# Kernel tuning notes

Hardware: AMD Instinct MI355X
Metric: run time of the kernel (lower is better)

Reference implementation:

```python
import jax, jax.numpy as jnp
import numpy as np

HID = 64      # hidden_dim
HEADS = 4     # attention heads
CH = HID // HEADS  # 16 per-head channels
EDIM = 6      # edge_dim
NEG = 0.2     # leaky_relu negative slope


def _glorot(key, shape):
    fan_in, fan_out = shape[0], shape[-1]
    s = np.sqrt(6.0 / (fan_in + fan_out)).astype(np.float32)
    return jax.random.uniform(key, shape, jnp.float32, -s, s)


def setup_inputs() -> dict:
    key = jax.random.key(0)
    ks = iter(jax.random.split(key, 48))
    N, E, T = 100000, 1200000, 20000
    inp = {
        "x": jax.random.normal(next(ks), (N, 7), jnp.float32),
        "pos": jax.random.normal(next(ks), (N, 3), jnp.float32),
        "node_type": jax.random.randint(next(ks), (N,), 0, 2),
        "edge_index": jax.random.randint(next(ks), (2, E), 0, N),
        "edge_attr": jax.random.normal(next(ks), (E, EDIM), jnp.float32),
        "num_tracks": T,
        "hidden_state": jax.random.normal(next(ks), (T, HID), jnp.float32),
        # params
        "type_emb": jax.random.normal(next(ks), (2, 8), jnp.float32),
        "enc_W1": _glorot(next(ks), (18, HID)), "enc_b1": jnp.zeros((HID,), jnp.float32),
        "enc_W2": _glorot(next(ks), (HID, HID)), "enc_b2": jnp.zeros((HID,), jnp.float32),
        "gru_Wi": _glorot(next(ks), (HID, 3 * HID)), "gru_bi": jnp.zeros((3 * HID,), jnp.float32),
        "gru_Wh": _glorot(next(ks), (HID, 3 * HID)), "gru_bh": jnp.zeros((3 * HID,), jnp.float32),
        "dec_W1": _glorot(next(ks), (HID, HID)), "dec_b1": jnp.zeros((HID,), jnp.float32),
        "dec_W2": _glorot(next(ks), (HID, 7)), "dec_b2": jnp.zeros((7,), jnp.float32),
    }
    for g in ("g1", "g2"):
        inp[g + "_Wl"] = _glorot(next(ks), (HID, HID))
        inp[g + "_bl"] = jnp.zeros((HID,), jnp.float32)
        inp[g + "_Wr"] = _glorot(next(ks), (HID, HID))
        inp[g + "_br"] = jnp.zeros((HID,), jnp.float32)
        inp[g + "_We"] = _glorot(next(ks), (EDIM, HID))
        inp[g + "_att"] = _glorot(next(ks), (HEADS, CH))
        inp[g + "_bias"] = jnp.zeros((HID,), jnp.float32)
    return inp


def _segment_softmax(e, seg, n):
    m = jax.ops.segment_max(e, seg, num_segments=n)
    m = jnp.where(jnp.isfinite(m), m, 0.0)
    ex = jnp.exp(e - m[seg])
    s = jax.ops.segment_sum(ex, seg, num_segments=n)
    return ex / (s[seg] + 1e-16)


def _gatv2(h, src, dst, eattr, Wl, bl, Wr, br, We, att, bias):
    N = h.shape[0]
    xl = (h @ Wl + bl).reshape(N, HEADS, CH)
    xr = (h @ Wr + br).reshape(N, HEADS, CH)
    ea = (eattr @ We).reshape(-1, HEADS, CH)
    g = jax.nn.leaky_relu(xl[src] + xr[dst] + ea, NEG)      # [E, H, C]
    e = jnp.einsum('ehc,hc->eh', g, att)                     # [E, H]
    alpha = _segment_softmax(e, dst, N)                      # [E, H]
    msg = xl[src] * alpha[..., None]                         # [E, H, C]
    out = jax.ops.segment_sum(msg, dst, num_segments=N)
    return out.reshape(N, HID) + bias, alpha


def reference(x, pos, node_type, edge_index, edge_attr, num_tracks, hidden_state,
              type_emb, enc_W1, enc_b1, enc_W2, enc_b2,
              g1_Wl, g1_bl, g1_Wr, g1_br, g1_We, g1_att, g1_bias,
              g2_Wl, g2_bl, g2_Wr, g2_br, g2_We, g2_att, g2_bias,
              gru_Wi, gru_bi, gru_Wh, gru_bh,
              dec_W1, dec_b1, dec_W2, dec_b2):
    N = x.shape[0]
    h = jnp.concatenate([x, pos, type_emb[node_type]], axis=-1)
    h = jax.nn.relu(h @ enc_W1 + enc_b1) @ enc_W2 + enc_b2

    # PyG GATv2Conv: add self loops, edge_attr fill_value='mean' (mean of incoming edges)
    src, dst = edge_index[0], edge_index[1]
    deg = jax.ops.segment_sum(jnp.ones(src.shape[0], jnp.float32), dst, num_segments=N)
    loop_attr = jax.ops.segment_sum(edge_attr, dst, num_segments=N) / jnp.maximum(deg, 1.0)[:, None]
    ar = jnp.arange(N)
    src_a = jnp.concatenate([src, ar])
    dst_a = jnp.concatenate([dst, ar])
    eattr_a = jnp.concatenate([edge_attr, loop_attr], axis=0)

    h1, a1 = _gatv2(h, src_a, dst_a, eattr_a, g1_Wl, g1_bl, g1_Wr, g1_br, g1_We, g1_att, g1_bias)
    h1 = jax.nn.relu(h1)
    h2, a2 = _gatv2(h1, src_a, dst_a, eattr_a, g2_Wl, g2_bl, g2_Wr, g2_br, g2_We, g2_att, g2_bias)

    # GRUCell on the first num_tracks nodes
    ht = h2[:num_tracks]
    gi = ht @ gru_Wi + gru_bi
    gh = hidden_state @ gru_Wh + gru_bh
    r = jax.nn.sigmoid(gi[:, :HID] + gh[:, :HID])
    z = jax.nn.sigmoid(gi[:, HID:2 * HID] + gh[:, HID:2 * HID])
    n = jnp.tanh(gi[:, 2 * HID:] + r * gh[:, 2 * HID:])
    new_tracks = (1.0 - z) * n + z * hidden_state

    new_full = jnp.concatenate([new_tracks, h2[num_tracks:]], axis=0)
    out = jax.nn.relu(new_full @ dec_W1 + dec_b1) @ dec_W2 + dec_b2  # [N, 7]
    final = out.at[:, :3].set(pos + out[:, :3])
    final = final.at[:, 3:6].set(x[:, :3] + out[:, 3:6])
    return final, new_full, a1, a2
```

## Files before the change

kernel.cpp:

```cpp
#include <hip/hip_runtime.h>

#define NEG 0.2f
#define LOG2E 1.44269504088896f
typedef unsigned short u16;

__device__ __forceinline__ float sigmoidf_(float v){ return 1.f/(1.f+__expf(-v)); }
__device__ __forceinline__ int rfl_(int v){ return __builtin_amdgcn_readfirstlane(v); }
__device__ __forceinline__ float bf2f_(unsigned u){ return __uint_as_float(u<<16); }
__device__ __forceinline__ u16 f2bf_(float f){
  unsigned u = __float_as_uint(f);
  u += 0x7FFFu + ((u>>16)&1u);
  return (u16)(u>>16);
}
template<int C>
__device__ __forceinline__ float dppadd_(float p){
  int r = __builtin_amdgcn_update_dpp(0, __float_as_int(p), C, 0xF, 0xF, true);
  return p + __int_as_float(r);
}
__device__ __forceinline__ float dppsum16_(float p){
  p = dppadd_<0x121>(p);
  p = dppadd_<0x122>(p);
  p = dppadd_<0x124>(p);
  p = dppadd_<0x128>(p);
  return p;
}

__global__ __launch_bounds__(256) void encdeg_kernel(
    const float* __restrict__ x, const float* __restrict__ pos,
    const int* __restrict__ ntype, const float* __restrict__ temb,
    const float* __restrict__ W1, const float* __restrict__ b1,
    const float* __restrict__ W2, const float* __restrict__ b2,
    float* __restrict__ hout,
    const int* __restrict__ ei, int* __restrict__ deg,
    int encB, int E, int N)
{
  __shared__ float sW1[18*64];
  __shared__ float sW2[4096];
  __shared__ float fT[4][8*20];
  __shared__ float tT[4][8*64];
  if ((int)blockIdx.x >= encB){
    int e = ((int)blockIdx.x - encB)*256 + threadIdx.x;
    if (e < E) atomicAdd(deg + ei[E+e], 1);
    return;
  }
  for (int i=threadIdx.x; i<18*64; i+=256) sW1[i]=W1[i];
  for (int i=threadIdx.x; i<4096; i+=256)  sW2[i]=W2[i];
  __syncthreads();
  int lane = threadIdx.x & 63;
  int wid  = threadIdx.x >> 6;
  int n0 = (blockIdx.x*4 + wid)*8;
  if (n0 >= N) return;
  float b1v=b1[lane], b2v=b2[lane];
  #pragma unroll
  for (int m=0;m<8;m++){
    int n=n0+m; float fv=0.f;
    if (n<N){
      if (lane<7)       fv=x[(size_t)n*7+lane];
      else if (lane<10) fv=pos[(size_t)n*3+lane-7];
      else if (lane<18) fv=temb[ntype[n]*8+lane-10];
    }
    if (lane<20) fT[wid][m*20+lane]=fv;
  }
  float t[8];
  #pragma unroll
  for (int m=0;m<8;m++) t[m]=b1v;
  #pragma unroll 2
  for (int k=0;k<18;k++){
    float w=sW1[k*64+lane];
    #pragma unroll
    for (int m=0;m<8;m++) t[m] += fT[wid][m*20+k]*w;
  }
  #pragma unroll
  for (int m=0;m<8;m++){ t[m]=fmaxf(t[m],0.f); tT[wid][m*64+lane]=t[m]; }
  float o[8];
  #pragma unroll
  for (int m=0;m<8;m++) o[m]=b2v;
  #pragma unroll 2
  for (int k=0;k<64;k++){
    float w=sW2[k*64+lane];
    #pragma unroll
    for (int m=0;m<8;m++) o[m] += tT[wid][m*64+k]*w;
  }
  #pragma unroll
  for (int m=0;m<8;m++){ int n=n0+m; if (n<N) hout[(size_t)n*64+lane]=o[m]; }
}

__global__ __launch_bounds__(256) void alloc_kernel(
    const int* __restrict__ deg, int* __restrict__ offs, int* __restrict__ counter, int N)
{
  __shared__ int wsum[4], woff[4], sbase;
  int lane = threadIdx.x & 63, w = threadIdx.x >> 6;
  int base = blockIdx.x*1024 + threadIdx.x*4;
  int v[4]; int s=0;
  #pragma unroll
  for (int j=0;j<4;j++){ int i=base+j; v[j]=(i<N)?deg[i]:0; s+=v[j]; }
  int inc=s;
  #pragma unroll
  for (int d=1;d<64;d<<=1){ int t=__shfl_up(inc,d); if (lane>=d) inc+=t; }
  if (lane==63) wsum[w]=inc;
  __syncthreads();
  if (threadIdx.x==0){
    woff[0]=0; woff[1]=wsum[0]; woff[2]=wsum[0]+wsum[1]; woff[3]=wsum[0]+wsum[1]+wsum[2];
    sbase = atomicAdd(counter, woff[3]+wsum[3]);
  }
  __syncthreads();
  int excl = sbase + woff[w] + (inc - s);
  #pragma unroll
  for (int j=0;j<4;j++){ int i=base+j; if (i<N) offs[i]=excl; excl+=v[j]; }
}

__global__ __launch_bounds__(256) void xfrmfill_kernel(
    const float* __restrict__ hin,
    const float* __restrict__ Wl, const float* __restrict__ bl,
    const float* __restrict__ Wr, const float* __restrict__ br,
    u16* __restrict__ xlo, u16* __restrict__ xro,
    const int* __restrict__ ei, const float* __restrict__ eattr,
    const int* __restrict__ offs,
    int* __restrict__ cursor, float4* __restrict__ slots,
    int xfB, int E, int N)
{
  __shared__ float hT[4][16*64];
  if ((int)blockIdx.x >= xfB){
    int e = ((int)blockIdx.x - xfB)*256 + threadIdx.x;
    if (e < E){
      int dst = ei[E + e];
      int p = atomicAdd(cursor + dst, 1);
      const float2* ep = (const float2*)(eattr + (size_t)e*6);
      float2 p0=ep[0], p1=ep[1], p2=ep[2];
      float4 a, b;
      a.x = __int_as_float(e); a.y = __int_as_float(ei[e]);
      a.z = p0.x; a.w = p0.y;
      b.x = p1.x; b.y = p1.y; b.z = p2.x; b.w = p2.y;
      unsigned slot = (unsigned)(offs[dst] + p);
      slots[slot*2u]   = a;
      slots[slot*2u+1] = b;
    }
    return;
  }
  int lane=threadIdx.x&63;
  int wid=threadIdx.x>>6;
  int n0=(blockIdx.x*4+wid)*16;
  if (n0>=N) return;
  #pragma unroll
  for (int m=0;m<16;m++){
    int n=n0+m;
    hT[wid][m*64+lane] = (n<N)? hin[(size_t)n*64+lane] : 0.f;
  }
  float blv=bl[lane], brv=br[lane];
  float al[16], ar[16];
  #pragma unroll
  for (int m=0;m<16;m++){ al[m]=blv; ar[m]=brv; }
  #pragma unroll 2
  for (int k=0;k<64;k++){
    float wl=Wl[k*64+lane], wr=Wr[k*64+lane];
    #pragma unroll
    for (int m=0;m<16;m++){
      float hb = hT[wid][m*64+k];
      al[m]+=hb*wl; ar[m]+=hb*wr;
    }
  }
  #pragma unroll
  for (int m=0;m<16;m++){
    int n=n0+m;
    if (n<N){ xlo[(((unsigned)n)<<6)+lane]=f2bf_(al[m]); xro[(((unsigned)n)<<6)+lane]=f2bf_(ar[m]); }
  }
}

__global__ __launch_bounds__(256) void xfrm_kernel(
    const float* __restrict__ hin,
    const float* __restrict__ Wl, const float* __restrict__ bl,
    const float* __restrict__ Wr, const float* __restrict__ br,
    u16* __restrict__ xlo, u16* __restrict__ xro, int N)
{
  __shared__ float sWl[4096], sWr[4096];
  __shared__ float hT[4][16*64];
  for (int i=threadIdx.x;i<4096;i+=256){ sWl[i]=Wl[i]; sWr[i]=Wr[i]; }
  __syncthreads();
  int lane=threadIdx.x&63;
  int wid=threadIdx.x>>6;
  int n0=(blockIdx.x*4+wid)*16;
  if (n0>=N) return;
  #pragma unroll
  for (int m=0;m<16;m++){
    int n=n0+m;
    hT[wid][m*64+lane] = (n<N)? hin[(size_t)n*64+lane] : 0.f;
  }
  float blv=bl[lane], brv=br[lane];
  float al[16], ar[16];
  #pragma unroll
  for (int m=0;m<16;m++){ al[m]=blv; ar[m]=brv; }
  #pragma unroll 2
  for (int k=0;k<64;k++){
    float wl=sWl[k*64+lane], wr=sWr[k*64+lane];
    #pragma unroll
    for (int m=0;m<16;m++){
      float hb = hT[wid][m*64+k];
      al[m]+=hb*wl; ar[m]+=hb*wr;
    }
  }
  #pragma unroll
  for (int m=0;m<16;m++){
    int n=n0+m;
    if (n<N){ xlo[(((unsigned)n)<<6)+lane]=f2bf_(al[m]); xro[(((unsigned)n)<<6)+lane]=f2bf_(ar[m]); }
  }
}

#define EDGE_STEP(EIDX, EADD, XV) do {                                       \
    float s_ = (XV) + xrv + (EADD);                                          \
    s_ = fmaxf(s_, NEG*s_);                                                  \
    float p_ = dppsum16_(s_*attv);                                           \
    if (isbase) aout[(((unsigned)(EIDX))<<2)+h] = p_;                        \
    if (__all(p_ <= mmax)) {                                                 \
      float w_ = exp2f(p_ - mmax);                                           \
      ssum += w_; acc += w_*(XV);                                            \
    } else {                                                                 \
      float mn_ = fmaxf(mmax, p_);                                           \
      float sc_ = exp2f(mmax - mn_);                                         \
      float w_  = exp2f(p_ - mn_);                                           \
      ssum = ssum*sc_ + w_;                                                  \
      acc  = acc*sc_ + w_*(XV);                                              \
      mmax = mn_;                                                            \
    }                                                                        \
  } while(0)

#define EDGE_PRE(J, OO) \
    float4 u##J = slots[(unsigned)(OO)*2u], v##J = slots[(unsigned)(OO)*2u+1u]; \
    int e##J = rfl_(__float_as_int(u##J.x)); \
    int s##J = rfl_(__float_as_int(u##J.y)); \
    unsigned xv##J = xlb[(((unsigned)s##J)<<6)+lane];

#define EDGE_BODY(J) \
    float d##J = u##J.z*we0 + u##J.w*we1 + v##J.x*we2 + v##J.y*we3 + v##J.z*we4 + v##J.w*we5; \
    dsum += d##J; \
    EDGE_STEP(e##J, d##J, bf2f_(xv##J));

__global__ __launch_bounds__(256) void gat_kernel(
    const float4* __restrict__ slots, const int* __restrict__ offs, const int* __restrict__ deg,
    const u16* __restrict__ xlb, const u16* __restrict__ xrb,
    const float* __restrict__ We, const float* __restrict__ att,
    const float* __restrict__ bias,
    float* __restrict__ aout, float2* __restrict__ msbuf,
    float* __restrict__ hout,
    int E, int N, int do_relu)
{
  int lane = threadIdx.x & 63;
  int n = blockIdx.x*4 + (threadIdx.x>>6);
  if (n >= N) return;
  float we0=We[lane], we1=We[64+lane], we2=We[128+lane],
        we3=We[192+lane], we4=We[256+lane], we5=We[320+lane];
  float attv = att[lane] * LOG2E;
  float bv = bias[lane];
  float xrv = bf2f_(xrb[(((unsigned)n)<<6)+lane]);
  int h = lane >> 4;
  bool isbase = (lane & 15) == 0;
  int o0 = rfl_(offs[n]);
  int dg = rfl_(deg[n]);
  int oend = o0 + dg;
  float mmax = -3.402823e38f, ssum=0.f, acc=0.f, dsum=0.f;
  int o = o0;
  for (; o+4 <= oend; o += 4){
    EDGE_PRE(0,o); EDGE_PRE(1,o+1); EDGE_PRE(2,o+2); EDGE_PRE(3,o+3);
    EDGE_BODY(0); EDGE_BODY(1); EDGE_BODY(2); EDGE_BODY(3);
  }
  for (; o < oend; ++o){
    EDGE_PRE(0,o);
    EDGE_BODY(0);
  }
  {
    float dS = dsum * (1.f/fmaxf((float)dg,1.f));
    float xvS = bf2f_((unsigned)xlb[(((unsigned)n)<<6)+lane]);
    EDGE_STEP(E+n, dS, xvS);
  }
  float sinv = 1.f/(ssum + 1e-16f);
  if (isbase) msbuf[(((unsigned)n)<<2)+h] = make_float2(mmax, sinv);
  float outv = acc*sinv + bv;
  if (do_relu) outv = fmaxf(outv, 0.f);
  hout[(((unsigned)n)<<6)+lane] = outv;
}

__global__ __launch_bounds__(256) void grudecalpha_kernel(
    const float* __restrict__ h2, const float* __restrict__ hid,
    const float* __restrict__ Wi, const float* __restrict__ bi,
    const float* __restrict__ Wh, const float* __restrict__ bh,
    const int* __restrict__ Tptr,
    const float* __restrict__ W1, const float* __restrict__ b1,
    const float* __restrict__ W2, const float* __restrict__ b2,
    const float* __restrict__ x, const float* __restrict__ pos,
    float* __restrict__ nf, float* __restrict__ fout,
    const int* __restrict__ ei,
    const float2* __restrict__ ms1, const float2* __restrict__ ms2,
    float4* __restrict__ a1, float4* __restrict__ a2,
    int gdB, int E, int N)
{
  __shared__ float sW1[4096];
  __shared__ float sW2[448];
  __shared__ float sb2[8];
  __shared__ float tT[4][8*68];
  __shared__ float pT[4][8*68];
  if ((int)blockIdx.x >= gdB){
    int e = ((int)blockIdx.x - gdB)*256 + threadIdx.x;
    if (e < E+N){
      int dst = (e<E)? ei[E+e] : (e-E);
      {
        float4 r = a1[e];
        const float2* mp = ms1 + (((unsigned)dst)<<2);
        float2 m0=mp[0], m1=mp[1], m2=mp[2], m3=mp[3];
        float4 o;
        o.x = exp2f(r.x - m0.x)*m0.y;
        o.y = exp2f(r.y - m1.x)*m1.y;
        o.z = exp2f(r.z - m2.x)*m2.y;
        o.w = exp2f(r.w - m3.x)*m3.y;
        a1[e] = o;
      }
      {
        float4 r = a2[e];
        const float2* mp = ms2 + (((unsigned)dst)<<2);
        float2 m0=mp[0], m1=mp[1], m2=mp[2], m3=mp[3];
        float4 o;
        o.x = exp2f(r.x - m0.x)*m0.y;
        o.y = exp2f(r.y - m1.x)*m1.y;
        o.z = exp2f(r.z - m2.x)*m2.y;
        o.w = exp2f(r.w - m3.x)*m3.y;
        a2[e] = o;
      }
    }
    return;
  }
  for (int i=threadIdx.x;i<4096;i+=256) sW1[i]=W1[i];
  for (int i=threadIdx.x;i<448;i+=256) sW2[i]=W2[i];
  if (threadIdx.x<7)  sb2[threadIdx.x]=b2[threadIdx.x];
  __syncthreads();
  int lane = threadIdx.x & 63;
  int wid  = threadIdx.x >> 6;
  int n0 = (blockIdx.x*4 + wid)*8;
  if (n0 >= N) return;
  int T = *Tptr;
  float hv[8], nfv[8];
  #pragma unroll
  for (int m=0;m<8;m++){ int n=n0+m; hv[m] = (n<N)? h2[(size_t)n*64+lane] : 0.f; }
  if (n0 < T){
    float pv[8];
    #pragma unroll
    for (int m=0;m<8;m++){ int n=n0+m; pv[m] = (n<T)? hid[(size_t)n*64+lane] : 0.f; }
    #pragma unroll
    for (int m=0;m<8;m++){ tT[wid][m*68+lane]=hv[m]; pT[wid][m*68+lane]=pv[m]; }
    float gr[8],gz[8],gn[8],hr[8],hz[8],hn[8];
    #pragma unroll
    for (int m=0;m<8;m++){ gr[m]=0.f;gz[m]=0.f;gn[m]=0.f;hr[m]=0.f;hz[m]=0.f;hn[m]=0.f; }
    for (int k=0;k<64;k++){
      float wir=Wi[k*192+lane], wiz=Wi[k*192+64+lane], win=Wi[k*192+128+lane];
      float whr=Wh[k*192+lane], whz=Wh[k*192+64+lane], whn=Wh[k*192+128+lane];
      #pragma unroll
      for (int m=0;m<8;m++){
        float a=tT[wid][m*68+k], b=pT[wid][m*68+k];
        gr[m]+=a*wir; gz[m]+=a*wiz; gn[m]+=a*win;
        hr[m]+=b*whr; hz[m]+=b*whz; hn[m]+=b*whn;
      }
    }
    float bir=bi[lane], biz=bi[64+lane], bin=bi[128+lane];
    float bhr=bh[lane], bhz=bh[64+lane], bhn=bh[128+lane];
    #pragma unroll
    for (int m=0;m<8;m++){
      int n=n0+m;
      if (n<T){
        float r  = sigmoidf_(gr[m]+bir + hr[m]+bhr);
        float z  = sigmoidf_(gz[m]+biz + hz[m]+bhz);
        float nn = tanhf(gn[m]+bin + r*(hn[m]+bhn));
        nfv[m] = (1.f-z)*nn + z*pv[m];
      } else {
        nfv[m] = hv[m];
      }
    }
  } else {
    #pragma unroll
    for (int m=0;m<8;m++) nfv[m] = hv[m];
  }
  #pragma unroll
  for (int m=0;m<8;m++){ int n=n0+m; if (n<N) nf[(size_t)n*64+lane]=nfv[m]; }
  #pragma unroll
  for (int m=0;m<8;m++) tT[wid][m*68+lane]=nfv[m];
  float t[8];
  float b1v=b1[lane];
  #pragma unroll
  for (int m=0;m<8;m++) t[m]=b1v;
  #pragma unroll 2
  for (int k=0;k<64;k++){
    float w=sW1[k*64+lane];
    #pragma unroll
    for (int m=0;m<8;m++) t[m] += tT[wid][m*68+k]*w;
  }
  #pragma unroll
  for (int m=0;m<8;m++) t[m]=fmaxf(t[m],0.f);
  #pragma unroll
  for (int m=0;m<8;m++) tT[wid][m*68+lane]=t[m];
  int mm = lane >> 3, cc = lane & 7;
  if (cc < 7){
    float a2v = sb2[cc];
    #pragma unroll 4
    for (int k=0;k<64;k++) a2v += tT[wid][mm*68+k]*sW2[k*7+cc];
    int n = n0+mm;
    if (n < N){
      if (cc<3)      a2v += pos[(size_t)n*3+cc];
      else if (cc<6) a2v += x[(size_t)n*7+(cc-3)];
      fout[(size_t)n*7+cc] = a2v;
    }
  }
}

extern "C" void kernel_launch(void* const* d_in, const int* in_sizes, int n_in,
                              void* d_out, int out_size, void* d_ws, size_t ws_size,
                              hipStream_t stream)
{
  const float* x     = (const float*)d_in[0];
  const float* pos   = (const float*)d_in[1];
  const int*   ntype = (const int*)d_in[2];
  const int*   eidx  = (const int*)d_in[3];
  const float* eattr = (const float*)d_in[4];
  const int*   Tptr  = (const int*)d_in[5];
  const float* hid   = (const float*)d_in[6];
  const float* temb  = (const float*)d_in[7];
  const float* encW1 = (const float*)d_in[8];
  const float* encb1 = (const float*)d_in[9];
  const float* encW2 = (const float*)d_in[10];
  const float* encb2 = (const float*)d_in[11];
  const float* gruWi = (const float*)d_in[12];
  const float* grubi = (const float*)d_in[13];
  const float* gruWh = (const float*)d_in[14];
  const float* grubh = (const float*)d_in[15];
  const float* decW1 = (const float*)d_in[16];
  const float* decb1 = (const float*)d_in[17];
  const float* decW2 = (const float*)d_in[18];
  const float* decb2 = (const float*)d_in[19];
  const float* gWl[2]  = {(const float*)d_in[20], (const float*)d_in[27]};
  const float* gbl[2]  = {(const float*)d_in[21], (const float*)d_in[28]};
  const float* gWr[2]  = {(const float*)d_in[22], (const float*)d_in[29]};
  const float* gbr[2]  = {(const float*)d_in[23], (const float*)d_in[30]};
  const float* gWe[2]  = {(const float*)d_in[24], (const float*)d_in[31]};
  const float* gatt[2] = {(const float*)d_in[25], (const float*)d_in[32]};
  const float* gbias[2]= {(const float*)d_in[26], (const float*)d_in[33]};

  int N  = in_sizes[0] / 7;
  int E  = in_sizes[3] / 2;
  int Ea = E + N;

  char* w = (char*)d_ws;
  float* A      = (float*)w; w += (size_t)N*64*sizeof(float);
  u16*   XL     = (u16*)w;  w += (size_t)N*64*sizeof(u16);
  u16*   XR     = (u16*)w;  w += (size_t)N*64*sizeof(u16);
  float2* msbuf1= (float2*)w; w += (size_t)N*4*sizeof(float2);
  float2* msbuf2= (float2*)w; w += (size_t)N*4*sizeof(float2);
  float4* slots = (float4*)w; w += (size_t)E*32;
  int*   deg    = (int*)w;   w += (size_t)N*sizeof(int);
  int*   cursor = (int*)w;   w += (size_t)N*sizeof(int);
  int*   counter= (int*)w;   w += 4*sizeof(int);
  int*   offs   = (int*)w;   w += (size_t)N*sizeof(int);

  float* out_final = (float*)d_out;
  float* out_nf    = out_final + (size_t)N*7;
  float* out_a1    = out_nf + (size_t)N*64;
  float* out_a2    = out_a1 + (size_t)Ea*4;

  hipMemsetAsync(deg, 0, ((size_t)2*N + 4)*sizeof(int), stream);

  int encB = (N+31)/32;
  int degB = (E+255)/256;
  encdeg_kernel<<<encB+degB, 256, 0, stream>>>(x,pos,ntype,temb,encW1,encb1,encW2,encb2,A,
      eidx, deg, encB, E, N);

  alloc_kernel<<<(N+1023)/1024, 256, 0, stream>>>(deg, offs, counter, N);

  int xfB = (N+63)/64;
  int flB = (E+255)/256;
  xfrmfill_kernel<<<xfB+flB, 256, 0, stream>>>(A, gWl[0], gbl[0], gWr[0], gbr[0], XL, XR,
      eidx, eattr, offs, cursor, slots, xfB, E, N);

  gat_kernel<<<(N+3)/4, 256, 0, stream>>>(slots, offs, deg, XL, XR,
      gWe[0], gatt[0], gbias[0], out_a1, msbuf1, A, E, N, 1);

  xfrm_kernel<<<xfB, 256, 0, stream>>>(A, gWl[1], gbl[1], gWr[1], gbr[1], XL, XR, N);
  gat_kernel<<<(N+3)/4, 256, 0, stream>>>(slots, offs, deg, XL, XR,
      gWe[1], gatt[1], gbias[1], out_a2, msbuf2, A, E, N, 0);

  int gdB = (N+31)/32;
  int alB = (Ea+255)/256;
  grudecalpha_kernel<<<gdB+alB, 256, 0, stream>>>(A, hid, gruWi, grubi, gruWh, grubh, Tptr,
      decW1, decb1, decW2, decb2, x, pos, out_nf, out_final,
      eidx, msbuf1, msbuf2, (float4*)out_a1, (float4*)out_a2, gdB, E, N);
}
```

Measured before the change: 509.1 us.

## Move layer-1 alpha normalization into xfrm kernel and seed cursor with offsets

The layer-1 attention normalization pass now runs as extra blocks inside the second transform kernel, so the final GRU/decoder kernel only normalizes layer-2 alphas and the two passes spread across two launches. The alloc kernel writes the prefix offsets straight into the cursor array, which lets the fill step take the slot index from the atomic and skip the offs[dst] lookup, and the memset shrinks. The xfrm and decoder kernels also stop staging weights in shared memory and read them from global/cache instead. This is meant to shorten the tail kernel and trim memory traffic, at the risk of slower uncached weight reads in the inner loops.

After: 499.1 us. -2.0%, faster.

```diff
diff --git a/kernel.cpp b/kernel.cpp
--- a/kernel.cpp
+++ b/kernel.cpp
@@ -23,6 +23,22 @@
   p = dppadd_<0x124>(p);
   p = dppadd_<0x128>(p);
   return p;
+}
+
+__device__ __forceinline__ void alpha_body_(int e, const int* __restrict__ ei,
+    const float2* __restrict__ ms, float4* __restrict__ a, int E, int N)
+{
+  if (e >= E+N) return;
+  int dst = (e<E)? ei[E+e] : (e-E);
+  float4 r = a[e];
+  const float2* mp = ms + (((unsigned)dst)<<2);
+  float2 m0=mp[0], m1=mp[1], m2=mp[2], m3=mp[3];
+  float4 o;
+  o.x = exp2f(r.x - m0.x)*m0.y;
+  o.y = exp2f(r.y - m1.x)*m1.y;
+  o.z = exp2f(r.z - m2.x)*m2.y;
+  o.w = exp2f(r.w - m3.x)*m3.y;
+  a[e] = o;
 }
 
 __global__ __launch_bounds__(256) void encdeg_kernel(
@@ -86,7 +102,8 @@
 }
 
 __global__ __launch_bounds__(256) void alloc_kernel(
-    const int* __restrict__ deg, int* __restrict__ offs, int* __restrict__ counter, int N)
+    const int* __restrict__ deg, int* __restrict__ offs, int* __restrict__ cursor,
+    int* __restrict__ counter, int N)
 {
   __shared__ int wsum[4], woff[4], sbase;
   int lane = threadIdx.x & 63, w = threadIdx.x >> 6;
@@ -106,7 +123,11 @@
   __syncthreads();
   int excl = sbase + woff[w] + (inc - s);
   #pragma unroll
-  for (int j=0;j<4;j++){ int i=base+j; if (i<N) offs[i]=excl; excl+=v[j]; }
+  for (int j=0;j<4;j++){
+    int i=base+j;
+    if (i<N){ offs[i]=excl; cursor[i]=excl; }
+    excl+=v[j];
+  }
 }
 
 __global__ __launch_bounds__(256) void xfrmfill_kernel(
@@ -115,7 +136,6 @@
     const float* __restrict__ Wr, const float* __restrict__ br,
     u16* __restrict__ xlo, u16* __restrict__ xro,
     const int* __restrict__ ei, const float* __restrict__ eattr,
-    const int* __restrict__ offs,
     int* __restrict__ cursor, float4* __restrict__ slots,
     int xfB, int E, int N)
 {
@@ -124,14 +144,13 @@
     int e = ((int)blockIdx.x - xfB)*256 + threadIdx.x;
     if (e < E){
       int dst = ei[E + e];
-      int p = atomicAdd(cursor + dst, 1);
+      unsigned slot = (unsigned)atomicAdd(cursor + dst, 1);
       const float2* ep = (const float2*)(eattr + (size_t)e*6);
       float2 p0=ep[0], p1=ep[1], p2=ep[2];
       float4 a, b;
       a.x = __int_as_float(e); a.y = __int_as_float(ei[e]);
       a.z = p0.x; a.w = p0.y;
       b.x = p1.x; b.y = p1.y; b.z = p2.x; b.w = p2.y;
-      unsigned slot = (unsigned)(offs[dst] + p);
       slots[slot*2u]   = a;
       slots[slot*2u+1] = b;
     }
@@ -166,16 +185,20 @@
   }
 }
 
-__global__ __launch_bounds__(256) void xfrm_kernel(
+__global__ __launch_bounds__(256) void xfrmalpha_kernel(
     const float* __restrict__ hin,
     const float* __restrict__ Wl, const float* __restrict__ bl,
     const float* __restrict__ Wr, const float* __restrict__ br,
-    u16* __restrict__ xlo, u16* __restrict__ xro, int N)
-{
-  __shared__ float sWl[4096], sWr[4096];
+    u16* __restrict__ xlo, u16* __restrict__ xro,
+    const int* __restrict__ ei, const float2* __restrict__ ms1, float4* __restrict__ a1,
+    int xfB, int E, int N)
+{
   __shared__ float hT[4][16*64];
-  for (int i=threadIdx.x;i<4096;i+=256){ sWl[i]=Wl[i]; sWr[i]=Wr[i]; }
-  __syncthreads();
+  if ((int)blockIdx.x >= xfB){
+    int e = ((int)blockIdx.x - xfB)*256 + threadIdx.x;
+    alpha_body_(e, ei, ms1, a1, E, N);
+    return;
+  }
   int lane=threadIdx.x&63;
   int wid=threadIdx.x>>6;
   int n0=(blockIdx.x*4+wid)*16;
@@ -191,7 +214,7 @@
   for (int m=0;m<16;m++){ al[m]=blv; ar[m]=brv; }
   #pragma unroll 2
   for (int k=0;k<64;k++){
-    float wl=sWl[k*64+lane], wr=sWr[k*64+lane];
+    float wl=Wl[k*64+lane], wr=Wr[k*64+lane];
     #pragma unroll
     for (int m=0;m<16;m++){
       float hb = hT[wid][m*64+k];
@@ -288,45 +311,18 @@
     const float* __restrict__ x, const float* __restrict__ pos,
     float* __restrict__ nf, float* __restrict__ fout,
     const int* __restrict__ ei,
-    const float2* __restrict__ ms1, const float2* __restrict__ ms2,
-    float4* __restrict__ a1, float4* __restrict__ a2,
+    const float2* __restrict__ ms2, float4* __restrict__ a2,
     int gdB, int E, int N)
 {
-  __shared__ float sW1[4096];
   __shared__ float sW2[448];
   __shared__ float sb2[8];
   __shared__ float tT[4][8*68];
   __shared__ float pT[4][8*68];
   if ((int)blockIdx.x >= gdB){
     int e = ((int)blockIdx.x - gdB)*256 + threadIdx.x;
-    if (e < E+N){
-      int dst = (e<E)? ei[E+e] : (e-E);
-      {
-        float4 r = a1[e];
-        const float2* mp = ms1 + (((unsigned)dst)<<2);
-        float2 m0=mp[0], m1=mp[1], m2=mp[2], m3=mp[3];
-        float4 o;
-        o.x = exp2f(r.x - m0.x)*m0.y;
-        o.y = exp2f(r.y - m1.x)*m1.y;
-        o.z = exp2f(r.z - m2.x)*m2.y;
-        o.w = exp2f(r.w - m3.x)*m3.y;
-        a1[e] = o;
-      }
-      {
-        float4 r = a2[e];
-        const float2* mp = ms2 + (((unsigned)dst)<<2);
-        float2 m0=mp[0], m1=mp[1], m2=mp[2], m3=mp[3];
-        float4 o;
-        o.x = exp2f(r.x - m0.x)*m0.y;
-        o.y = exp2f(r.y - m1.x)*m1.y;
-        o.z = exp2f(r.z - m2.x)*m2.y;
-        o.w = exp2f(r.w - m3.x)*m3.y;
-        a2[e] = o;
-      }
-    }
+    alpha_body_(e, ei, ms2, a2, E, N);
     return;
   }
-  for (int i=threadIdx.x;i<4096;i+=256) sW1[i]=W1[i];
   for (int i=threadIdx.x;i<448;i+=256) sW2[i]=W2[i];
   if (threadIdx.x<7)  sb2[threadIdx.x]=b2[threadIdx.x];
   __syncthreads();
@@ -385,7 +381,7 @@
   for (int m=0;m<8;m++) t[m]=b1v;
   #pragma unroll 2
   for (int k=0;k<64;k++){
-    float w=sW1[k*64+lane];
+    float w=W1[k*64+lane];
     #pragma unroll
     for (int m=0;m<8;m++) t[m] += tT[wid][m*68+k]*w;
   }
@@ -451,8 +447,8 @@
   float2* msbuf2= (float2*)w; w += (size_t)N*4*sizeof(float2);
   float4* slots = (float4*)w; w += (size_t)E*32;
   int*   deg    = (int*)w;   w += (size_t)N*sizeof(int);
+  int*   counter= (int*)w;   w += 4*sizeof(int);
   int*   cursor = (int*)w;   w += (size_t)N*sizeof(int);
-  int*   counter= (int*)w;   w += 4*sizeof(int);
   int*   offs   = (int*)w;   w += (size_t)N*sizeof(int);
 
   float* out_final = (float*)d_out;
@@ -460,30 +456,32 @@
   float* out_a1    = out_nf + (size_t)N*64;
   float* out_a2    = out_a1 + (size_t)Ea*4;
 
-  hipMemsetAsync(deg, 0, ((size_t)2*N + 4)*sizeof(int), stream);
+  hipMemsetAsync(deg, 0, ((size_t)N + 4)*sizeof(int), stream);
 
   int encB = (N+31)/32;
   int degB = (E+255)/256;
   encdeg_kernel<<<encB+degB, 256, 0, stream>>>(x,pos,ntype,temb,encW1,encb1,encW2,encb2,A,
       eidx, deg, encB, E, N);
 
-  alloc_kernel<<<(N+1023)/1024, 256, 0, stream>>>(deg, offs, counter, N);
+  alloc_kernel<<<(N+1023)/1024, 256, 0, stream>>>(deg, offs, cursor, counter, N);
 
   int xfB = (N+63)/64;
   int flB = (E+255)/256;
   xfrmfill_kernel<<<xfB+flB, 256, 0, stream>>>(A, gWl[0], gbl[0], gWr[0], gbr[0], XL, XR,
-      eidx, eattr, offs, cursor, slots, xfB, E, N);
+      eidx, eattr, cursor, slots, xfB, E, N);
 
   gat_kernel<<<(N+3)/4, 256, 0, stream>>>(slots, offs, deg, XL, XR,
       gWe[0], gatt[0], gbias[0], out_a1, msbuf1, A, E, N, 1);
 
-  xfrm_kernel<<<xfB, 256, 0, stream>>>(A, gWl[1], gbl[1], gWr[1], gbr[1], XL, XR, N);
+  int alB = (Ea+255)/256;
+  xfrmalpha_kernel<<<xfB+alB, 256, 0, stream>>>(A, gWl[1], gbl[1], gWr[1], gbr[1], XL, XR,
+      eidx, msbuf1, (float4*)out_a1, xfB, E, N);
+
   gat_kernel<<<(N+3)/4, 256, 0, stream>>>(slots, offs, deg, XL, XR,
       gWe[1], gatt[1], gbias[1], out_a2, msbuf2, A, E, N, 0);
 
   int gdB = (N+31)/32;
-  int alB = (Ea+255)/256;
   grudecalpha_kernel<<<gdB+alB, 256, 0, stream>>>(A, hid, gruWi, grubi, gruWh, grubh, Tptr,
       decW1, decb1, decW2, decb2, x, pos, out_nf, out_final,
-      eidx, msbuf1, msbuf2, (float4*)out_a1, (float4*)out_a2, gdB, E, N);
-}
+      eidx, msbuf2, (float4*)out_a2, gdB, E, N);
+}
```

## Seed scatter cursors with CSR offsets and batch edges per thread

Applied to the files above, without the earlier changes.

The alloc kernel now writes each node's exclusive offset into the cursor array too, so the fill pass gets the slot straight from the atomicAdd without an extra offs[dst] gather. The cursor array no longer needs zeroing, so the memset shrinks. The degree-count and fill blocks each handle four edges per thread, which cuts the number of blocks. The decoder kernel stops staging W1 in shared memory and reads it from global/cache, which trades a block-wide load for per-iteration global reads.

Result: no change. 515.5 us (+1.3%).

```diff
diff --git a/kernel.cpp b/kernel.cpp
--- a/kernel.cpp
+++ b/kernel.cpp
@@ -39,8 +39,12 @@
   __shared__ float fT[4][8*20];
   __shared__ float tT[4][8*64];
   if ((int)blockIdx.x >= encB){
-    int e = ((int)blockIdx.x - encB)*256 + threadIdx.x;
-    if (e < E) atomicAdd(deg + ei[E+e], 1);
+    int base = ((int)blockIdx.x - encB)*1024 + (int)threadIdx.x;
+    #pragma unroll
+    for (int j=0;j<4;j++){
+      int e = base + j*256;
+      if (e < E) atomicAdd(deg + ei[E+e], 1);
+    }
     return;
   }
   for (int i=threadIdx.x; i<18*64; i+=256) sW1[i]=W1[i];
@@ -86,7 +90,8 @@
 }
 
 __global__ __launch_bounds__(256) void alloc_kernel(
-    const int* __restrict__ deg, int* __restrict__ offs, int* __restrict__ counter, int N)
+    const int* __restrict__ deg, int* __restrict__ offs, int* __restrict__ cursor,
+    int* __restrict__ counter, int N)
 {
   __shared__ int wsum[4], woff[4], sbase;
   int lane = threadIdx.x & 63, w = threadIdx.x >> 6;
@@ -106,7 +111,11 @@
   __syncthreads();
   int excl = sbase + woff[w] + (inc - s);
   #pragma unroll
-  for (int j=0;j<4;j++){ int i=base+j; if (i<N) offs[i]=excl; excl+=v[j]; }
+  for (int j=0;j<4;j++){
+    int i=base+j;
+    if (i<N){ offs[i]=excl; cursor[i]=excl; }
+    excl+=v[j];
+  }
 }
 
 __global__ __launch_bounds__(256) void xfrmfill_kernel(
@@ -115,25 +124,27 @@
     const float* __restrict__ Wr, const float* __restrict__ br,
     u16* __restrict__ xlo, u16* __restrict__ xro,
     const int* __restrict__ ei, const float* __restrict__ eattr,
-    const int* __restrict__ offs,
     int* __restrict__ cursor, float4* __restrict__ slots,
     int xfB, int E, int N)
 {
   __shared__ float hT[4][16*64];
   if ((int)blockIdx.x >= xfB){
-    int e = ((int)blockIdx.x - xfB)*256 + threadIdx.x;
-    if (e < E){
-      int dst = ei[E + e];
-      int p = atomicAdd(cursor + dst, 1);
-      const float2* ep = (const float2*)(eattr + (size_t)e*6);
-      float2 p0=ep[0], p1=ep[1], p2=ep[2];
-      float4 a, b;
-      a.x = __int_as_float(e); a.y = __int_as_float(ei[e]);
-      a.z = p0.x; a.w = p0.y;
-      b.x = p1.x; b.y = p1.y; b.z = p2.x; b.w = p2.y;
-      unsigned slot = (unsigned)(offs[dst] + p);
-      slots[slot*2u]   = a;
-      slots[slot*2u+1] = b;
+    int base = ((int)blockIdx.x - xfB)*1024 + (int)threadIdx.x;
+    #pragma unroll
+    for (int j=0;j<4;j++){
+      int e = base + j*256;
+      if (e < E){
+        int dst = ei[E + e];
+        unsigned slot = (unsigned)atomicAdd(cursor + dst, 1);
+        const float2* ep = (const float2*)(eattr + (size_t)e*6);
+        float2 p0=ep[0], p1=ep[1], p2=ep[2];
+        float4 a, b;
+        a.x = __int_as_float(e); a.y = __int_as_float(ei[e]);
+        a.z = p0.x; a.w = p0.y;
+        b.x = p1.x; b.y = p1.y; b.z = p2.x; b.w = p2.y;
+        slots[slot*2u]   = a;
+        slots[slot*2u+1] = b;
+      }
     }
     return;
   }
@@ -292,13 +303,12 @@
     float4* __restrict__ a1, float4* __restrict__ a2,
     int gdB, int E, int N)
 {
-  __shared__ float sW1[4096];
   __shared__ float sW2[448];
   __shared__ float sb2[8];
   __shared__ float tT[4][8*68];
   __shared__ float pT[4][8*68];
   if ((int)blockIdx.x >= gdB){
-    int e = ((int)blockIdx.x - gdB)*256 + threadIdx.x;
+    int e = ((int)blockIdx.x - gdB)*256 + (int)threadIdx.x;
     if (e < E+N){
       int dst = (e<E)? ei[E+e] : (e-E);
       {
@@ -326,7 +336,6 @@
     }
     return;
   }
-  for (int i=threadIdx.x;i<4096;i+=256) sW1[i]=W1[i];
   for (int i=threadIdx.x;i<448;i+=256) sW2[i]=W2[i];
   if (threadIdx.x<7)  sb2[threadIdx.x]=b2[threadIdx.x];
   __syncthreads();
@@ -385,7 +394,7 @@
   for (int m=0;m<8;m++) t[m]=b1v;
   #pragma unroll 2
   for (int k=0;k<64;k++){
-    float w=sW1[k*64+lane];
+    float w=W1[k*64+lane];
     #pragma unroll
     for (int m=0;m<8;m++) t[m] += tT[wid][m*68+k]*w;
   }
@@ -451,8 +460,8 @@
   float2* msbuf2= (float2*)w; w += (size_t)N*4*sizeof(float2);
   float4* slots = (float4*)w; w += (size_t)E*32;
   int*   deg    = (int*)w;   w += (size_t)N*sizeof(int);
+  int*   counter= (int*)w;   w += 4*sizeof(int);
   int*   cursor = (int*)w;   w += (size_t)N*sizeof(int);
-  int*   counter= (int*)w;   w += 4*sizeof(int);
   int*   offs   = (int*)w;   w += (size_t)N*sizeof(int);
 
   float* out_final = (float*)d_out;
@@ -460,25 +469,27 @@
   float* out_a1    = out_nf + (size_t)N*64;
   float* out_a2    = out_a1 + (size_t)Ea*4;
 
-  hipMemsetAsync(deg, 0, ((size_t)2*N + 4)*sizeof(int), stream);
+  hipMemsetAsync(deg, 0, ((size_t)N + 4)*sizeof(int), stream);
 
   int encB = (N+31)/32;
-  int degB = (E+255)/256;
+  int degB = (E+1023)/1024;
   encdeg_kernel<<<encB+degB, 256, 0, stream>>>(x,pos,ntype,temb,encW1,encb1,encW2,encb2,A,
       eidx, deg, encB, E, N);
 
-  alloc_kernel<<<(N+1023)/1024, 256, 0, stream>>>(deg, offs, counter, N);
+  alloc_kernel<<<(N+1023)/1024, 256, 0, stream>>>(deg, offs, cursor, counter, N);
 
   int xfB = (N+63)/64;
-  int flB = (E+255)/256;
+  int flB = (E+1023)/1024;
   xfrmfill_kernel<<<xfB+flB, 256, 0, stream>>>(A, gWl[0], gbl[0], gWr[0], gbr[0], XL, XR,
-      eidx, eattr, offs, cursor, slots, xfB, E, N);
-
-  gat_kernel<<<(N+3)/4, 256, 0, stream>>>(slots, offs, deg, XL, XR,
+      eidx, eattr, cursor, slots, xfB, E, N);
+
+  int gatB = (N+3)/4;
+  gat_kernel<<<gatB, 256, 0, stream>>>(slots, offs, deg, XL, XR,
       gWe[0], gatt[0], gbias[0], out_a1, msbuf1, A, E, N, 1);
 
   xfrm_kernel<<<xfB, 256, 0, stream>>>(A, gWl[1], gbl[1], gWr[1], gbr[1], XL, XR, N);
-  gat_kernel<<<(N+3)/4, 256, 0, stream>>>(slots, offs, deg, XL, XR,
+
+  gat_kernel<<<gatB, 256, 0, stream>>>(slots, offs, deg, XL, XR,
       gWe[1], gatt[1], gbias[1], out_a2, msbuf2, A, E, N, 0);
 
   int gdB = (N+31)/32;
```
